# Optimization experiments

Measured on AMD Instinct MI355X. Metric: run time of the kernel, lower is better.

Reference implementation:

```python
import jax, jax.numpy as jnp
import numpy as np

N = 8192          # num nodes
F = 256           # feature_size
D = 128           # graph_embedding_size
E = 262144        # num edges (avg degree 32)
SLOPE = 0.2       # cfg.negativeslope
NEG_INF = -9e15   # matches torch's -9000000000000000.0 mask value


def setup_inputs() -> dict:
    key = jax.random.key(0)
    k1, k2, k3, k4 = jax.random.split(key, 4)
    X = jax.random.normal(k1, (N, F), dtype=jnp.float32)
    edge_index = jax.random.randint(k2, (2, E), 0, N, dtype=jnp.int64)
    # glorot init for Ws, xavier_uniform(gain=1.414) for a
    lim_ws = np.sqrt(6.0 / (F + D)).astype(np.float32)
    Ws = jax.random.uniform(k3, (F, D), jnp.float32, -lim_ws, lim_ws)
    lim_a = (1.414 * np.sqrt(6.0 / (2 * D + 1))).astype(np.float32)
    a = jax.random.uniform(k4, (2 * D, 1), jnp.float32, -lim_a, lim_a)
    return {"edge_index": edge_index, "X": X, "Ws": Ws, "a": a}


def reference(edge_index, X, Ws, a):
    # dense adjacency mask from edge list (sparse_coo_tensor(...).to_dense())
    adj = jnp.zeros((N, N), jnp.float32).at[edge_index[0], edge_index[1]].set(1.0)
    Wh = X @ Ws                                   # [N, D]
    # GAT-style score: Wh1_i + Wh2_j, then leaky relu
    e = jax.nn.leaky_relu(Wh @ a[:D] + (Wh @ a[D:]).T, SLOPE)  # [N, N]
    scores = jnp.where(adj > 0, e, NEG_INF)
    att = jax.nn.softmax(scores, axis=1)          # masked row softmax
    return jax.nn.elu(att @ Wh)                   # [N, D]
```

## Files before the change

kernel.cpp:

```cpp
#include <hip/hip_runtime.h>
#include <math.h>

#define N_NODES 8192
#define FDIM 256
#define DDIM 128
#define SLOPE 0.2f
#define MAXD 128
#define RSL 32
#define NREP 8

typedef __attribute__((ext_vector_type(8))) short bf16x8;
typedef __attribute__((ext_vector_type(4))) float f32x4;

__device__ __forceinline__ unsigned short f2bf(float f) {
    unsigned u = __float_as_uint(f);
    u += 0x7fffu + ((u >> 16) & 1u);
    return (unsigned short)(u >> 16);
}
__device__ __forceinline__ float bf2f(unsigned short h) {
    return __uint_as_float(((unsigned)h) << 16);
}

__global__ __launch_bounds__(256) void prep_k(const float* __restrict__ Ws,
                                              unsigned short* __restrict__ Bphi,
                                              unsigned short* __restrict__ Bplo,
                                              unsigned* __restrict__ cnt8) {
    int b = blockIdx.x, t = threadIdx.x;
    int zi = b * 256 + t;
    if (zi < NREP * N_NODES / 4) ((uint4*)cnt8)[zi] = make_uint4(0u, 0u, 0u, 0u);

    if (b >= 16) return;
    int tid = b * 256 + t;
    int ct = tid >> 9, ks = (tid >> 6) & 7, l = tid & 63;
    int kbase = ks * 32 + (l >> 4) * 8;
    int col = ct * 16 + (l & 15);
    bf16x8 h, lo;
#pragma unroll
    for (int q = 0; q < 8; q++) {
        float v = Ws[(size_t)(kbase + q) * DDIM + col];
        unsigned short hq = f2bf(v);
        h[q] = (short)hq;
        lo[q] = (short)f2bf(v - bf2f(hq));
    }
    *(bf16x8*)(Bphi + (size_t)tid * 8) = h;
    *(bf16x8*)(Bplo + (size_t)tid * 8) = lo;
}

__global__ __launch_bounds__(256) void mega_k(const int* __restrict__ edge, int E,
                                              const float* __restrict__ X,
                                              const unsigned short* __restrict__ Bphi,
                                              const unsigned short* __restrict__ Bplo,
                                              const float* __restrict__ a,
                                              unsigned short* __restrict__ WhB,
                                              float* __restrict__ s1,
                                              float* __restrict__ s2,
                                              unsigned* __restrict__ cnt8,
                                              unsigned* __restrict__ ell8) {
    __shared__ unsigned short Ah[16 * 264], Al[16 * 264];
    __shared__ float ps1[64], ps2[64];
    int bid = blockIdx.x, t = threadIdx.x;

    if (bid >= 512) {
        unsigned xcd;
        asm volatile("s_getreg_b32 %0, hwreg(HW_REG_XCC_ID)" : "=s"(xcd));
        xcd &= 7u;
        int e = (bid - 512) * 256 + t;
        if (e < E) {
            int r = edge[e];
            int c = edge[E + e];
            size_t rowk = (size_t)xcd * N_NODES + (unsigned)r;
            unsigned slot = atomicAdd(&cnt8[rowk], 1u);
            if (slot < RSL) ell8[rowk * RSL + slot] = (unsigned)c;
        }
        return;
    }

    int w = t >> 6, lane = t & 63, lr = lane & 15, kg = lane >> 4;
    int row0 = bid * 16;

    const float4* Xg = (const float4*)(X + (size_t)row0 * FDIM);
#pragma unroll
    for (int i = 0; i < 4; i++) {
        int lin = t + 256 * i;
        int r = lin >> 6, q = lin & 63;
        float4 v = Xg[r * 64 + q];
        ushort4 h, l;
        h.x = f2bf(v.x); l.x = f2bf(v.x - bf2f(h.x));
        h.y = f2bf(v.y); l.y = f2bf(v.y - bf2f(h.y));
        h.z = f2bf(v.z); l.z = f2bf(v.z - bf2f(h.z));
        h.w = f2bf(v.w); l.w = f2bf(v.w - bf2f(h.w));
        *(ushort4*)(Ah + r * 264 + q * 4) = h;
        *(ushort4*)(Al + r * 264 + q * 4) = l;
    }
    __syncthreads();

    f32x4 acc0 = (f32x4){0.f, 0.f, 0.f, 0.f};
    f32x4 acc1 = (f32x4){0.f, 0.f, 0.f, 0.f};
    int ct0 = 2 * w, ct1 = 2 * w + 1;

#pragma unroll 2
    for (int ks = 0; ks < 8; ks++) {
        bf16x8 ahi = *(bf16x8*)(Ah + lr * 264 + ks * 32 + kg * 8);
        bf16x8 alo = *(bf16x8*)(Al + lr * 264 + ks * 32 + kg * 8);
        size_t o0 = (size_t)((ct0 * 8 + ks) * 64 + lane) * 8;
        size_t o1 = (size_t)((ct1 * 8 + ks) * 64 + lane) * 8;
        bf16x8 bh0 = *(const bf16x8*)(Bphi + o0);
        bf16x8 bl0 = *(const bf16x8*)(Bplo + o0);
        bf16x8 bh1 = *(const bf16x8*)(Bphi + o1);
        bf16x8 bl1 = *(const bf16x8*)(Bplo + o1);
        acc0 = __builtin_amdgcn_mfma_f32_16x16x32_bf16(ahi, bh0, acc0, 0, 0, 0);
        acc0 = __builtin_amdgcn_mfma_f32_16x16x32_bf16(ahi, bl0, acc0, 0, 0, 0);
        acc0 = __builtin_amdgcn_mfma_f32_16x16x32_bf16(alo, bh0, acc0, 0, 0, 0);
        acc1 = __builtin_amdgcn_mfma_f32_16x16x32_bf16(ahi, bh1, acc1, 0, 0, 0);
        acc1 = __builtin_amdgcn_mfma_f32_16x16x32_bf16(ahi, bl1, acc1, 0, 0, 0);
        acc1 = __builtin_amdgcn_mfma_f32_16x16x32_bf16(alo, bh1, acc1, 0, 0, 0);
    }

#pragma unroll
    for (int r = 0; r < 4; r++) {
        int row = row0 + kg * 4 + r;
        int c0 = ct0 * 16 + lr, c1 = ct1 * 16 + lr;
        float v0 = acc0[r], v1 = acc1[r];
        WhB[(size_t)row * DDIM + c0] = f2bf(v0);
        WhB[(size_t)row * DDIM + c1] = f2bf(v1);
        float q1 = v0 * a[c0] + v1 * a[c1];
        float q2 = v0 * a[DDIM + c0] + v1 * a[DDIM + c1];
        for (int o = 1; o < 16; o <<= 1) {
            q1 += __shfl_xor(q1, o, 16);
            q2 += __shfl_xor(q2, o, 16);
        }
        if (lr == 0) { ps1[w * 16 + kg * 4 + r] = q1; ps2[w * 16 + kg * 4 + r] = q2; }
    }
    __syncthreads();
    if (t < 16) {
        s1[row0 + t] = (ps1[t] + ps1[16 + t]) + (ps1[32 + t] + ps1[48 + t]);
        s2[row0 + t] = (ps2[t] + ps2[16 + t]) + (ps2[32 + t] + ps2[48 + t]);
    }
}

__global__ __launch_bounds__(256) void row_wave_k(const unsigned* __restrict__ cnt8,
                                                  const unsigned* __restrict__ ell8,
                                                  const float* __restrict__ s1v,
                                                  const float* __restrict__ s2v,
                                                  const unsigned short* __restrict__ WhB,
                                                  float* __restrict__ out) {
    __shared__ unsigned bmw[4][256];
    __shared__ float    pe[4][MAXD];
    __shared__ unsigned jl[4][MAXD];
    __shared__ unsigned lcnt[4];

    int w = threadIdx.x >> 6, lane = threadIdx.x & 63;
    int i = blockIdx.x * 4 + w;
    const ushort2* WhB2 = (const ushort2*)WhB;

    ((uint4*)bmw[w])[lane] = make_uint4(0u, 0u, 0u, 0u);
    if (lane == 0) lcnt[w] = 0u;
    float s1i = s1v[i];
    float lmax = -3e38f;

#pragma unroll
    for (int k = 0; k < NREP; k++) {
        size_t rowk = (size_t)k * N_NODES + i;
        unsigned dk = cnt8[rowk];
        if (dk > RSL) dk = RSL;
        if (lane < (int)dk) {
            unsigned j = ell8[rowk * RSL + lane];
            unsigned m = 1u << (j & 31);
            unsigned old = atomicOr(&bmw[w][j >> 5], m);
            if (!(old & m)) {
                float e = s1i + s2v[j];
                e = e > 0.f ? e : SLOPE * e;
                lmax = fmaxf(lmax, e);
                unsigned pos = atomicAdd(&lcnt[w], 1u);
                if (pos < MAXD) { jl[w][pos] = j; pe[w][pos] = e; }
            }
        }
    }
    for (int o = 32; o; o >>= 1) lmax = fmaxf(lmax, __shfl_xor(lmax, o, 64));
    unsigned deg = lcnt[w];
    if (deg > MAXD) deg = MAXD;

    if (deg == 0u) {
        float sx = 0.f, sy = 0.f;
        for (int rr = 0; rr < N_NODES; rr++) {
            ushort2 u = WhB2[(size_t)rr * 64 + lane];
            sx += bf2f(u.x); sy += bf2f(u.y);
        }
        sx *= (1.0f / N_NODES); sy *= (1.0f / N_NODES);
        sx = sx > 0.f ? sx : __expf(sx) - 1.f;
        sy = sy > 0.f ? sy : __expf(sy) - 1.f;
        ((float2*)out)[(size_t)i * 64 + lane] = make_float2(sx, sy);
        return;
    }

    float lsum = 0.f;
    for (unsigned n = lane; n < deg; n += 64) {
        float p = __expf(pe[w][n] - lmax);
        pe[w][n] = p;
        lsum += p;
    }
    for (int o = 32; o; o >>= 1) lsum += __shfl_xor(lsum, o, 64);
    float inv = 1.0f / lsum;

    float ax = 0.f, ay = 0.f;
#pragma unroll 8
    for (unsigned n = 0; n < deg; ++n) {
        float p = pe[w][n];
        unsigned j = jl[w][n];
        ushort2 u = WhB2[(size_t)j * 64 + lane];
        ax = fmaf(p, bf2f(u.x), ax);
        ay = fmaf(p, bf2f(u.y), ay);
    }
    ax *= inv; ay *= inv;
    ax = ax > 0.f ? ax : __expf(ax) - 1.f;
    ay = ay > 0.f ? ay : __expf(ay) - 1.f;
    ((float2*)out)[(size_t)i * 64 + lane] = make_float2(ax, ay);
}

extern "C" void kernel_launch(void* const* d_in, const int* in_sizes, int n_in,
                              void* d_out, int out_size, void* d_ws, size_t ws_size,
                              hipStream_t stream) {
    const int*   edge = (const int*)d_in[0];
    const float* X    = (const float*)d_in[1];
    const float* Ws   = (const float*)d_in[2];
    const float* a    = (const float*)d_in[3];
    float*       out  = (float*)d_out;
    int E = in_sizes[0] / 2;

    char* ws = (char*)d_ws;
    size_t off = 0;
    unsigned*       cnt8 = (unsigned*)(ws + off); off += (size_t)NREP * N_NODES * 4;
    unsigned*       ell8 = (unsigned*)(ws + off); off += (size_t)NREP * N_NODES * RSL * 4;
    float*          s1   = (float*)(ws + off);    off += N_NODES * 4;
    float*          s2   = (float*)(ws + off);    off += N_NODES * 4;
    unsigned short* WhB  = (unsigned short*)(ws + off); off += (size_t)N_NODES * DDIM * 2;
    unsigned short* Bphi = (unsigned short*)(ws + off); off += (size_t)FDIM * DDIM * 2;
    unsigned short* Bplo = (unsigned short*)(ws + off); off += (size_t)FDIM * DDIM * 2;

    int nbuild = (E + 255) / 256;
    prep_k<<<256, 256, 0, stream>>>(Ws, Bphi, Bplo, cnt8);
    mega_k<<<512 + nbuild, 256, 0, stream>>>(edge, E, X, Bphi, Bplo, a, WhB, s1, s2, cnt8, ell8);
    row_wave_k<<<N_NODES / 4, 256, 0, stream>>>(cnt8, ell8, s1, s2, WhB, out);
}
```

Before: 44.53 us.

## Replace global-atomic ELL adjacency build with per-block LDS bucketed edge segments

```diff
diff --git a/kernel.cpp b/kernel.cpp
--- a/kernel.cpp
+++ b/kernel.cpp
@@ -6,8 +6,10 @@
 #define DDIM 128
 #define SLOPE 0.2f
 #define MAXD 128
-#define RSL 32
-#define NREP 8
+#define NBKT 256
+#define CELLU 16
+#define CAP 15
+#define EPB 512
 
 typedef __attribute__((ext_vector_type(8))) short bf16x8;
 typedef __attribute__((ext_vector_type(4))) float f32x4;
@@ -23,14 +25,8 @@
 
 __global__ __launch_bounds__(256) void prep_k(const float* __restrict__ Ws,
                                               unsigned short* __restrict__ Bphi,
-                                              unsigned short* __restrict__ Bplo,
-                                              unsigned* __restrict__ cnt8) {
-    int b = blockIdx.x, t = threadIdx.x;
-    int zi = b * 256 + t;
-    if (zi < NREP * N_NODES / 4) ((uint4*)cnt8)[zi] = make_uint4(0u, 0u, 0u, 0u);
-
-    if (b >= 16) return;
-    int tid = b * 256 + t;
+                                              unsigned short* __restrict__ Bplo) {
+    int tid = blockIdx.x * 256 + threadIdx.x;
     int ct = tid >> 9, ks = (tid >> 6) & 7, l = tid & 63;
     int kbase = ks * 32 + (l >> 4) * 8;
     int col = ct * 16 + (l & 15);
@@ -54,24 +50,33 @@
                                               unsigned short* __restrict__ WhB,
                                               float* __restrict__ s1,
                                               float* __restrict__ s2,
-                                              unsigned* __restrict__ cnt8,
-                                              unsigned* __restrict__ ell8) {
+                                              unsigned* __restrict__ seg) {
     __shared__ unsigned short Ah[16 * 264], Al[16 * 264];
     __shared__ float ps1[64], ps2[64];
+    __shared__ unsigned hcnt[NBKT];
     int bid = blockIdx.x, t = threadIdx.x;
 
     if (bid >= 512) {
-        unsigned xcd;
-        asm volatile("s_getreg_b32 %0, hwreg(HW_REG_XCC_ID)" : "=s"(xcd));
-        xcd &= 7u;
-        int e = (bid - 512) * 256 + t;
-        if (e < E) {
-            int r = edge[e];
-            int c = edge[E + e];
-            size_t rowk = (size_t)xcd * N_NODES + (unsigned)r;
-            unsigned slot = atomicAdd(&cnt8[rowk], 1u);
-            if (slot < RSL) ell8[rowk * RSL + slot] = (unsigned)c;
-        }
+        int hb = bid - 512;
+        hcnt[t] = 0u;
+        __syncthreads();
+#pragma unroll
+        for (int it = 0; it < EPB / 256; ++it) {
+            int e = hb * EPB + it * 256 + t;
+            if (e < E) {
+                int r = edge[e];
+                int c = edge[E + e];
+                int q = r >> 5;
+                unsigned rank = atomicAdd(&hcnt[q], 1u);
+                if (rank < CAP)
+                    seg[((size_t)hb * NBKT + q) * CELLU + 1 + rank] =
+                        (unsigned)c | ((unsigned)(r & 31) << 13);
+            }
+        }
+        __syncthreads();
+        unsigned cq = hcnt[t];
+        if (cq > CAP) cq = CAP;
+        seg[((size_t)hb * NBKT + t) * CELLU] = cq;
         return;
     }
 
@@ -138,8 +143,7 @@
     }
 }
 
-__global__ __launch_bounds__(256) void row_wave_k(const unsigned* __restrict__ cnt8,
-                                                  const unsigned* __restrict__ ell8,
+__global__ __launch_bounds__(256) void row_wave_k(const unsigned* __restrict__ seg, int nhb,
                                                   const float* __restrict__ s1v,
                                                   const float* __restrict__ s2v,
                                                   const unsigned short* __restrict__ WhB,
@@ -152,27 +156,66 @@
     int w = threadIdx.x >> 6, lane = threadIdx.x & 63;
     int i = blockIdx.x * 4 + w;
     const ushort2* WhB2 = (const ushort2*)WhB;
+    const uint4* seg4 = (const uint4*)seg;
 
     ((uint4*)bmw[w])[lane] = make_uint4(0u, 0u, 0u, 0u);
     if (lane == 0) lcnt[w] = 0u;
+    int q = i >> 5, rlt = i & 31;
     float s1i = s1v[i];
     float lmax = -3e38f;
 
-#pragma unroll
-    for (int k = 0; k < NREP; k++) {
-        size_t rowk = (size_t)k * N_NODES + i;
-        unsigned dk = cnt8[rowk];
-        if (dk > RSL) dk = RSL;
-        if (lane < (int)dk) {
-            unsigned j = ell8[rowk * RSL + lane];
-            unsigned m = 1u << (j & 31);
-            unsigned old = atomicOr(&bmw[w][j >> 5], m);
-            if (!(old & m)) {
-                float e = s1i + s2v[j];
-                e = e > 0.f ? e : SLOPE * e;
-                lmax = fmaxf(lmax, e);
-                unsigned pos = atomicAdd(&lcnt[w], 1u);
-                if (pos < MAXD) { jl[w][pos] = j; pe[w][pos] = e; }
+    for (int k = 0; k < 8; ++k) {
+        int b = lane + (k << 6);
+        if (b >= nhb) break;
+        size_t cb = ((size_t)b * NBKT + q) * (CELLU / 4);
+        uint4 v = seg4[cb];
+        unsigned cnt = v.x;
+        if (cnt > CAP) cnt = CAP;
+        unsigned done = 0;
+        unsigned cur[4] = {0u, v.y, v.z, v.w};
+        int have = 3, idx = 1;
+        while (done < cnt) {
+            int take = (int)(cnt - done) < have ? (int)(cnt - done) : have;
+#pragma unroll
+            for (int x = 0; x < 3; ++x) {
+                if (x < take) {
+                    unsigned word = cur[x + (have == 3 ? 1 : 0)];
+                    unsigned rl = (word >> 13) & 31u;
+                    if (rl == (unsigned)rlt) {
+                        unsigned j = word & 8191u;
+                        unsigned m = 1u << (j & 31);
+                        unsigned old = atomicOr(&bmw[w][j >> 5], m);
+                        if (!(old & m)) {
+                            float e = s1i + s2v[j];
+                            e = e > 0.f ? e : SLOPE * e;
+                            lmax = fmaxf(lmax, e);
+                            unsigned pos = atomicAdd(&lcnt[w], 1u);
+                            if (pos < MAXD) { jl[w][pos] = j; pe[w][pos] = e; }
+                        }
+                    }
+                }
+            }
+            if (have == 4 && take == 4) {
+                unsigned word = cur[3];
+                unsigned rl = (word >> 13) & 31u;
+                if (rl == (unsigned)rlt) {
+                    unsigned j = word & 8191u;
+                    unsigned m = 1u << (j & 31);
+                    unsigned old = atomicOr(&bmw[w][j >> 5], m);
+                    if (!(old & m)) {
+                        float e = s1i + s2v[j];
+                        e = e > 0.f ? e : SLOPE * e;
+                        lmax = fmaxf(lmax, e);
+                        unsigned pos = atomicAdd(&lcnt[w], 1u);
+                        if (pos < MAXD) { jl[w][pos] = j; pe[w][pos] = e; }
+                    }
+                }
+            }
+            done += take;
+            if (done < cnt) {
+                uint4 v2 = seg4[cb + idx]; ++idx;
+                cur[0] = v2.x; cur[1] = v2.y; cur[2] = v2.z; cur[3] = v2.w;
+                have = 4;
             }
         }
     }
@@ -226,19 +269,18 @@
     const float* a    = (const float*)d_in[3];
     float*       out  = (float*)d_out;
     int E = in_sizes[0] / 2;
+    int nhb = (E + EPB - 1) / EPB;
 
     char* ws = (char*)d_ws;
     size_t off = 0;
-    unsigned*       cnt8 = (unsigned*)(ws + off); off += (size_t)NREP * N_NODES * 4;
-    unsigned*       ell8 = (unsigned*)(ws + off); off += (size_t)NREP * N_NODES * RSL * 4;
+    unsigned*       seg  = (unsigned*)(ws + off); off += (size_t)nhb * NBKT * CELLU * 4;
     float*          s1   = (float*)(ws + off);    off += N_NODES * 4;
     float*          s2   = (float*)(ws + off);    off += N_NODES * 4;
     unsigned short* WhB  = (unsigned short*)(ws + off); off += (size_t)N_NODES * DDIM * 2;
     unsigned short* Bphi = (unsigned short*)(ws + off); off += (size_t)FDIM * DDIM * 2;
     unsigned short* Bplo = (unsigned short*)(ws + off); off += (size_t)FDIM * DDIM * 2;
 
-    int nbuild = (E + 255) / 256;
-    prep_k<<<256, 256, 0, stream>>>(Ws, Bphi, Bplo, cnt8);
-    mega_k<<<512 + nbuild, 256, 0, stream>>>(edge, E, X, Bphi, Bplo, a, WhB, s1, s2, cnt8, ell8);
-    row_wave_k<<<N_NODES / 4, 256, 0, stream>>>(cnt8, ell8, s1, s2, WhB, out);
-}
+    prep_k<<<16, 256, 0, stream>>>(Ws, Bphi, Bplo);
+    mega_k<<<512 + nhb, 256, 0, stream>>>(edge, E, X, Bphi, Bplo, a, WhB, s1, s2, seg);
+    row_wave_k<<<N_NODES / 4, 256, 0, stream>>>(seg, nhb, s1, s2, WhB, out);
+}
```

After: 60.81 us. 1.37x slower.

## Bucket edges with LDS histograms per edge chunk instead of global atomics

Applied to the files above, without the earlier changes.

```diff
diff --git a/kernel.cpp b/kernel.cpp
--- a/kernel.cpp
+++ b/kernel.cpp
@@ -6,8 +6,10 @@
 #define DDIM 128
 #define SLOPE 0.2f
 #define MAXD 128
-#define RSL 32
-#define NREP 8
+#define NHB 32
+#define EPB 8192
+#define CAP 7
+#define OVW 16
 
 typedef __attribute__((ext_vector_type(8))) short bf16x8;
 typedef __attribute__((ext_vector_type(4))) float f32x4;
@@ -24,13 +26,10 @@
 __global__ __launch_bounds__(256) void prep_k(const float* __restrict__ Ws,
                                               unsigned short* __restrict__ Bphi,
                                               unsigned short* __restrict__ Bplo,
-                                              unsigned* __restrict__ cnt8) {
-    int b = blockIdx.x, t = threadIdx.x;
-    int zi = b * 256 + t;
-    if (zi < NREP * N_NODES / 4) ((uint4*)cnt8)[zi] = make_uint4(0u, 0u, 0u, 0u);
-
-    if (b >= 16) return;
-    int tid = b * 256 + t;
+                                              unsigned* __restrict__ ovCnt) {
+    int tid = blockIdx.x * 256 + threadIdx.x;
+    ovCnt[tid * 2] = 0u;
+    ovCnt[tid * 2 + 1] = 0u;
     int ct = tid >> 9, ks = (tid >> 6) & 7, l = tid & 63;
     int kbase = ks * 32 + (l >> 4) * 8;
     int col = ct * 16 + (l & 15);
@@ -54,27 +53,46 @@
                                               unsigned short* __restrict__ WhB,
                                               float* __restrict__ s1,
                                               float* __restrict__ s2,
-                                              unsigned* __restrict__ cnt8,
-                                              unsigned* __restrict__ ell8) {
-    __shared__ unsigned short Ah[16 * 264], Al[16 * 264];
+                                              unsigned* __restrict__ seg,
+                                              unsigned* __restrict__ ovCnt,
+                                              unsigned* __restrict__ ovEll) {
+    __shared__ char smem[16896];
     __shared__ float ps1[64], ps2[64];
     int bid = blockIdx.x, t = threadIdx.x;
 
     if (bid >= 512) {
-        unsigned xcd;
-        asm volatile("s_getreg_b32 %0, hwreg(HW_REG_XCC_ID)" : "=s"(xcd));
-        xcd &= 7u;
-        int e = (bid - 512) * 256 + t;
-        if (e < E) {
-            int r = edge[e];
-            int c = edge[E + e];
-            size_t rowk = (size_t)xcd * N_NODES + (unsigned)r;
-            unsigned slot = atomicAdd(&cnt8[rowk], 1u);
-            if (slot < RSL) ell8[rowk * RSL + slot] = (unsigned)c;
+        unsigned* hcnt = (unsigned*)smem;
+        int hb = bid - 512;
+        for (int i = t; i < 4096; i += 256) hcnt[i] = 0u;
+        __syncthreads();
+#pragma unroll
+        for (int it = 0; it < EPB / 256; ++it) {
+            int e = hb * EPB + it * 256 + t;
+            if (e < E) {
+                int r = edge[e];
+                int c = edge[E + e];
+                unsigned sh = (r & 1) << 4;
+                unsigned old = atomicAdd(&hcnt[r >> 1], 1u << sh);
+                unsigned rank = (old >> sh) & 0xffffu;
+                if (rank < CAP) {
+                    seg[((size_t)hb * N_NODES + r) * 8 + 1 + rank] = (unsigned)c;
+                } else {
+                    unsigned s = atomicAdd(&ovCnt[r], 1u);
+                    if (s < OVW) ovEll[(size_t)r * OVW + s] = (unsigned)c;
+                }
+            }
+        }
+        __syncthreads();
+        for (int rr = t; rr < N_NODES; rr += 256) {
+            unsigned cnt = (hcnt[rr >> 1] >> ((rr & 1) << 4)) & 0xffffu;
+            if (cnt > CAP) cnt = CAP;
+            seg[((size_t)hb * N_NODES + rr) * 8] = cnt;
         }
         return;
     }
 
+    unsigned short* Ah = (unsigned short*)smem;
+    unsigned short* Al = Ah + 16 * 264;
     int w = t >> 6, lane = t & 63, lr = lane & 15, kg = lane >> 4;
     int row0 = bid * 16;
 
@@ -138,8 +156,9 @@
     }
 }
 
-__global__ __launch_bounds__(256) void row_wave_k(const unsigned* __restrict__ cnt8,
-                                                  const unsigned* __restrict__ ell8,
+__global__ __launch_bounds__(256) void row_wave_k(const unsigned* __restrict__ seg,
+                                                  const unsigned* __restrict__ ovCnt,
+                                                  const unsigned* __restrict__ ovEll,
                                                   const float* __restrict__ s1v,
                                                   const float* __restrict__ s2v,
                                                   const unsigned short* __restrict__ WhB,
@@ -158,24 +177,53 @@
     float s1i = s1v[i];
     float lmax = -3e38f;
 
-#pragma unroll
-    for (int k = 0; k < NREP; k++) {
-        size_t rowk = (size_t)k * N_NODES + i;
-        unsigned dk = cnt8[rowk];
-        if (dk > RSL) dk = RSL;
-        if (lane < (int)dk) {
-            unsigned j = ell8[rowk * RSL + lane];
-            unsigned m = 1u << (j & 31);
-            unsigned old = atomicOr(&bmw[w][j >> 5], m);
-            if (!(old & m)) {
-                float e = s1i + s2v[j];
-                e = e > 0.f ? e : SLOPE * e;
-                lmax = fmaxf(lmax, e);
-                unsigned pos = atomicAdd(&lcnt[w], 1u);
-                if (pos < MAXD) { jl[w][pos] = j; pe[w][pos] = e; }
-            }
-        }
-    }
+    unsigned e0w = 0, e1w = 0, e2w = 0, e3w = 0, e4w = 0, e5w = 0, e6w = 0;
+    unsigned cnt = 0;
+    if (lane < NHB) {
+        const uint4* c4 = (const uint4*)(seg + ((size_t)lane * N_NODES + i) * 8);
+        uint4 v0 = c4[0];
+        cnt = v0.x > CAP ? CAP : v0.x;
+        e0w = v0.y; e1w = v0.z; e2w = v0.w;
+        if (cnt > 3) {
+            uint4 v1 = c4[1];
+            e3w = v1.x; e4w = v1.y; e5w = v1.z; e6w = v1.w;
+        }
+    }
+    unsigned od = ovCnt[i];
+    if (od > OVW) od = OVW;
+
+    {
+        unsigned wl0 = e0w, wl1 = e1w, wl2 = e2w, wl3 = e3w, wl4 = e4w, wl5 = e5w, wl6 = e6w;
+#define PROC(WORD, X)                                                          \
+        if ((X) < (int)cnt) {                                                  \
+            unsigned j = (WORD) & 8191u;                                       \
+            unsigned m = 1u << (j & 31);                                       \
+            unsigned old = atomicOr(&bmw[w][j >> 5], m);                       \
+            if (!(old & m)) {                                                  \
+                float e = s1i + s2v[j];                                        \
+                e = e > 0.f ? e : SLOPE * e;                                   \
+                lmax = fmaxf(lmax, e);                                         \
+                unsigned pos = atomicAdd(&lcnt[w], 1u);                        \
+                if (pos < MAXD) { jl[w][pos] = j; pe[w][pos] = e; }            \
+            }                                                                  \
+        }
+        PROC(wl0, 0) PROC(wl1, 1) PROC(wl2, 2) PROC(wl3, 3)
+        PROC(wl4, 4) PROC(wl5, 5) PROC(wl6, 6)
+#undef PROC
+    }
+    if (lane < (int)od) {
+        unsigned j = ovEll[(size_t)i * OVW + lane] & 8191u;
+        unsigned m = 1u << (j & 31);
+        unsigned old = atomicOr(&bmw[w][j >> 5], m);
+        if (!(old & m)) {
+            float e = s1i + s2v[j];
+            e = e > 0.f ? e : SLOPE * e;
+            lmax = fmaxf(lmax, e);
+            unsigned pos = atomicAdd(&lcnt[w], 1u);
+            if (pos < MAXD) { jl[w][pos] = j; pe[w][pos] = e; }
+        }
+    }
+
     for (int o = 32; o; o >>= 1) lmax = fmaxf(lmax, __shfl_xor(lmax, o, 64));
     unsigned deg = lcnt[w];
     if (deg > MAXD) deg = MAXD;
@@ -229,16 +277,17 @@
 
     char* ws = (char*)d_ws;
     size_t off = 0;
-    unsigned*       cnt8 = (unsigned*)(ws + off); off += (size_t)NREP * N_NODES * 4;
-    unsigned*       ell8 = (unsigned*)(ws + off); off += (size_t)NREP * N_NODES * RSL * 4;
-    float*          s1   = (float*)(ws + off);    off += N_NODES * 4;
-    float*          s2   = (float*)(ws + off);    off += N_NODES * 4;
-    unsigned short* WhB  = (unsigned short*)(ws + off); off += (size_t)N_NODES * DDIM * 2;
-    unsigned short* Bphi = (unsigned short*)(ws + off); off += (size_t)FDIM * DDIM * 2;
-    unsigned short* Bplo = (unsigned short*)(ws + off); off += (size_t)FDIM * DDIM * 2;
-
-    int nbuild = (E + 255) / 256;
-    prep_k<<<256, 256, 0, stream>>>(Ws, Bphi, Bplo, cnt8);
-    mega_k<<<512 + nbuild, 256, 0, stream>>>(edge, E, X, Bphi, Bplo, a, WhB, s1, s2, cnt8, ell8);
-    row_wave_k<<<N_NODES / 4, 256, 0, stream>>>(cnt8, ell8, s1, s2, WhB, out);
-}
+    unsigned*       seg   = (unsigned*)(ws + off); off += (size_t)NHB * N_NODES * 8 * 4;
+    unsigned*       ovCnt = (unsigned*)(ws + off); off += N_NODES * 4;
+    unsigned*       ovEll = (unsigned*)(ws + off); off += (size_t)N_NODES * OVW * 4;
+    float*          s1    = (float*)(ws + off);    off += N_NODES * 4;
+    float*          s2    = (float*)(ws + off);    off += N_NODES * 4;
+    unsigned short* WhB   = (unsigned short*)(ws + off); off += (size_t)N_NODES * DDIM * 2;
+    unsigned short* Bphi  = (unsigned short*)(ws + off); off += (size_t)FDIM * DDIM * 2;
+    unsigned short* Bplo  = (unsigned short*)(ws + off); off += (size_t)FDIM * DDIM * 2;
+
+    prep_k<<<16, 256, 0, stream>>>(Ws, Bphi, Bplo, ovCnt);
+    mega_k<<<512 + NHB, 256, 0, stream>>>(edge, E, X, Bphi, Bplo, a, WhB, s1, s2,
+                                          seg, ovCnt, ovEll);
+    row_wave_k<<<N_NODES / 4, 256, 0, stream>>>(seg, ovCnt, ovEll, s1, s2, WhB, out);
+}
```

Measured after the change: 44.56 us. About the same (+0.1%).
